# Kernel tuning notes

Hardware: AMD Instinct MI355X
Metric: run time of the kernel (lower is better)

## Reference

```python
import jax, jax.numpy as jnp
import numpy as np

N_SPK, N_UTT, D = 512, 64, 1024
EPS = 1e-6  # matches tf.math.l2_normalize default epsilon guard


def _l2norm(x, axis=-1):
    return x / jnp.sqrt(jnp.maximum(jnp.sum(x * x, axis=axis, keepdims=True), EPS))


def setup_inputs() -> dict:
    key = jax.random.key(0)
    k1, _ = jax.random.split(key)
    inputs = jax.random.normal(k1, (N_SPK, N_UTT, D), dtype=jnp.float32)
    w = jnp.asarray(10.0, dtype=jnp.float32)
    b = jnp.asarray(-5.0, dtype=jnp.float32)
    return {"inputs": inputs, "w": w, "b": b}


def reference(inputs, w, b):
    N, M, _ = inputs.shape
    # speaker centroids: mean over utterances -> [N, D]
    centroids = jnp.mean(inputs, axis=1)
    # utterance (exclusion) centroids: mean of the other M-1 utterances -> [N, M, D]
    ut_centroids = (jnp.sum(inputs, axis=1, keepdims=True) - inputs) / (M - 1)

    e = _l2norm(inputs)          # [N, M, D]
    c = _l2norm(centroids)       # [N, D]
    uc = _l2norm(ut_centroids)   # [N, M, D]

    # cosine sim of every utterance vs every speaker centroid -> [N, M, K]
    cos_all = jnp.einsum('nmd,kd->nmk', e, c)
    # same-speaker entries use the self-exclusion centroid
    cos_self = jnp.sum(e * uc, axis=-1)  # [N, M]
    eye = jnp.eye(N, dtype=inputs.dtype)[:, None, :]  # [N, 1, N]
    cos_sim = cos_all * (1.0 - eye) + cos_self[:, :, None] * eye

    sim = w * cos_sim + b  # [N, M, N]
    # softmax contrastive loss: -S_{j,i,j} + logsumexp_k S_{j,i,k}, summed
    lse = jax.nn.logsumexp(sim, axis=-1)            # [N, M]
    pos = jnp.einsum('nmn->nm', sim)                # diagonal along speaker axes
    loss = jnp.sum(lse - pos)
    return loss
```

## Files before the change

### kernel.cpp

```cpp
#include <hip/hip_runtime.h>
#include <stdint.h>

#define N_SPK 512
#define N_UTT 64
#define DIM   1024
#define NROWS (N_SPK * N_UTT)
#define EPS   1e-6f

#define BM2 256
#define BN2 256
#define BK2 32
#define KT2 (DIM / BK2)

typedef __attribute__((ext_vector_type(8))) short short8;
typedef __attribute__((ext_vector_type(4))) float f32x4;

__device__ __forceinline__ uint16_t f2bf(float f) {
    union { float f; uint32_t i; } un; un.f = f;
    uint32_t x = un.i;
    return (uint16_t)((x + 0x7fffu + ((x >> 16) & 1u)) >> 16);
}

__global__ __launch_bounds__(256) void prep_centroid(
    const float* __restrict__ x, uint16_t* __restrict__ xb,
    uint16_t* __restrict__ cmat, float* __restrict__ xxg,
    float* __restrict__ ssqg)
{
    const int n    = blockIdx.x;
    const int tid  = threadIdx.x;
    const int lane = tid & 63;
    const int w    = tid >> 6;

    const float* xn  = x  + (size_t)n * N_UTT * DIM;
    uint16_t*    xbn = xb + (size_t)n * N_UTT * DIM;

    float Sp[16];
    #pragma unroll
    for (int j = 0; j < 16; ++j) Sp[j] = 0.f;

    #pragma unroll 1
    for (int o = 0; o < 4; ++o) {
        const int m0 = w * 16 + o * 4;

        float4 v[16];
        #pragma unroll
        for (int i = 0; i < 4; ++i)
            #pragma unroll
            for (int j = 0; j < 4; ++j)
                v[i * 4 + j] = *(const float4*)(xn + (size_t)(m0 + i) * DIM + j * 256 + lane * 4);

        float xx[4] = {0.f, 0.f, 0.f, 0.f};
        #pragma unroll
        for (int i = 0; i < 4; ++i) {
            #pragma unroll
            for (int j = 0; j < 4; ++j) {
                const float4 qv = v[i * 4 + j];
                xx[i] += qv.x * qv.x + qv.y * qv.y + qv.z * qv.z + qv.w * qv.w;
                Sp[j * 4 + 0] += qv.x; Sp[j * 4 + 1] += qv.y;
                Sp[j * 4 + 2] += qv.z; Sp[j * 4 + 3] += qv.w;
                ushort4 ov;
                ov.x = f2bf(qv.x); ov.y = f2bf(qv.y); ov.z = f2bf(qv.z); ov.w = f2bf(qv.w);
                *(ushort4*)(xbn + (size_t)(m0 + i) * DIM + j * 256 + lane * 4) = ov;
            }
        }

        #pragma unroll
        for (int i = 0; i < 4; ++i) {
            float t = xx[i];
            #pragma unroll
            for (int off = 1; off < 64; off <<= 1) t += __shfl_xor(t, off);
            if (lane == 0) xxg[n * N_UTT + m0 + i] = t;
        }
    }

    __shared__ float Sh[4][DIM];
    #pragma unroll
    for (int j = 0; j < 4; ++j)
        *(float4*)&Sh[w][j * 256 + lane * 4] =
            make_float4(Sp[j * 4], Sp[j * 4 + 1], Sp[j * 4 + 2], Sp[j * 4 + 3]);
    __syncthreads();

    const int d0 = tid * 4;
    float4 S  = *(const float4*)&Sh[0][d0];
    const float4 b1 = *(const float4*)&Sh[1][d0];
    const float4 b2 = *(const float4*)&Sh[2][d0];
    const float4 b3 = *(const float4*)&Sh[3][d0];
    S.x += b1.x + b2.x + b3.x; S.y += b1.y + b2.y + b3.y;
    S.z += b1.z + b2.z + b3.z; S.w += b1.w + b2.w + b3.w;

    float css = S.x * S.x + S.y * S.y + S.z * S.z + S.w * S.w;
    #pragma unroll
    for (int off = 1; off < 64; off <<= 1) css += __shfl_xor(css, off);
    __shared__ float red[4];
    if ((tid & 63) == 0) red[tid >> 6] = css;
    __syncthreads();
    const float ssq = red[0] + red[1] + red[2] + red[3];

    const float scale = rsqrtf(fmaxf(ssq * (1.0f / 4096.f), EPS)) * (1.0f / 64.f);
    ushort4 oc;
    oc.x = f2bf(S.x * scale); oc.y = f2bf(S.y * scale);
    oc.z = f2bf(S.z * scale); oc.w = f2bf(S.w * scale);
    *(ushort4*)(cmat + (size_t)n * DIM + d0) = oc;
    if (tid == 0) ssqg[n] = ssq;
}

__global__ __launch_bounds__(512, 2) void gemm_lse_kernel(
    const uint16_t* __restrict__ xb, const uint16_t* __restrict__ cmat,
    const float* __restrict__ xxg, const float* __restrict__ ssqg,
    const float* __restrict__ wp, const float* __restrict__ bp,
    float* __restrict__ sumexp2, float* __restrict__ pos)
{
    __shared__ char smem[65536];
    uint16_t* As = (uint16_t*)smem;
    uint16_t* Bs = (uint16_t*)(smem + 32768);
    float*    Se = (float*)smem;

    const int tid   = threadIdx.x;
    const int lane  = tid & 63;
    const int wid   = tid >> 6;
    const int waveM = wid >> 2;
    const int waveN = wid & 3;

    const int bid = blockIdx.x;
    const int rt  = bid & 127;
    const int ct  = bid >> 7;

    const int rowBase = rt * BM2;
    const int colBase = ct * BN2;

    const uint16_t* gAp[2];
    const uint16_t* gBp[2];
    int ldso[2];
    #pragma unroll
    for (int i = 0; i < 2; ++i) {
        const int s    = i * 512 + tid;
        const int srow = s >> 2;
        const int kc   = (s & 3) ^ (srow & 3);
        gAp[i]  = xb   + (size_t)(rowBase + srow) * DIM + kc * 8;
        gBp[i]  = cmat + (size_t)(colBase + srow) * DIM + kc * 8;
        ldso[i] = s * 16;
    }

#define STAGE(buf, ko)                                                          \
    {                                                                           \
        _Pragma("unroll")                                                       \
        for (int i_ = 0; i_ < 2; ++i_) {                                        \
            __builtin_amdgcn_global_load_lds(                                   \
                (const __attribute__((address_space(1))) void*)(gAp[i_] + (ko)),\
                (__attribute__((address_space(3))) void*)(smem + (buf) * 16384 + ldso[i_]), \
                16, 0, 0);                                                      \
            __builtin_amdgcn_global_load_lds(                                   \
                (const __attribute__((address_space(1))) void*)(gBp[i_] + (ko)),\
                (__attribute__((address_space(3))) void*)(smem + 32768 + (buf) * 16384 + ldso[i_]), \
                16, 0, 0);                                                      \
        }                                                                       \
    }

    f32x4 acc[8][4];
    #pragma unroll
    for (int i = 0; i < 8; ++i)
        #pragma unroll
        for (int j = 0; j < 4; ++j)
            acc[i][j] = (f32x4){0.f, 0.f, 0.f, 0.f};

    const int cL = lane & 15;
    const int q  = lane >> 4;

    STAGE(0, 0);
    __syncthreads();

    int cur = 0;
    for (int kt = 0; kt < KT2; ++kt) {
        if (kt + 1 < KT2) STAGE(cur ^ 1, (kt + 1) * BK2);

        const uint16_t* Ab = As + cur * (256 * 32);
        const uint16_t* Bb = Bs + cur * (256 * 32);

        short8 a[8], b[4];
        #pragma unroll
        for (int bi = 0; bi < 8; ++bi) {
            const int row = waveM * 128 + bi * 16 + cL;
            const int ch  = q ^ (row & 3);
            a[bi] = *(const short8*)&Ab[row * 32 + ch * 8];
        }
        #pragma unroll
        for (int bj = 0; bj < 4; ++bj) {
            const int row = waveN * 64 + bj * 16 + cL;
            const int ch  = q ^ (row & 3);
            b[bj] = *(const short8*)&Bb[row * 32 + ch * 8];
        }

        #pragma unroll
        for (int bi = 0; bi < 8; ++bi)
            #pragma unroll
            for (int bj = 0; bj < 4; ++bj)
                acc[bi][bj] = __builtin_amdgcn_mfma_f32_16x16x32_bf16(
                    a[bi], b[bj], acc[bi][bj], 0, 0, 0);

        __syncthreads();
        cur ^= 1;
    }
#undef STAGE

    const float wv = wp[0], bv = bp[0];
    #pragma unroll
    for (int bi = 0; bi < 8; ++bi) {
        #pragma unroll
        for (int r = 0; r < 4; ++r) {
            const int R     = rowBase + waveM * 128 + bi * 16 + q * 4 + r;
            const float xxv = xxg[R];
            const float rn  = rsqrtf(fmaxf(xxv, EPS));
            const int nrow  = R >> 6;
            float s = 0.f;
            #pragma unroll
            for (int bj = 0; bj < 4; ++bj) {
                const int col = colBase + waveN * 64 + bj * 16 + cL;
                const float dot = acc[bi][bj][r];
                float sim;
                if (col == nrow) {
                    const float ssqv = ssqg[nrow];
                    const float xs   = dot * sqrtf(ssqv);
                    const float d2   = ssqv - 2.f * xs + xxv;
                    const float cs   = ((xs - xxv) * (1.f / 63.f)) * rn *
                                       rsqrtf(fmaxf(d2 * (1.f / 3969.f), EPS));
                    sim = wv * cs + bv;
                    pos[R] = sim;
                } else {
                    sim = wv * (dot * rn) + bv;
                }
                s += __expf(sim);
            }
            #pragma unroll
            for (int off = 1; off < 16; off <<= 1) s += __shfl_xor(s, off);
            if (cL == 0)
                Se[waveN * 256 + waveM * 128 + bi * 16 + q * 4 + r] = s;
        }
    }
    __syncthreads();
    if (tid < 256) {
        const float t = Se[tid] + Se[256 + tid] + Se[512 + tid] + Se[768 + tid];
        sumexp2[(size_t)ct * NROWS + rowBase + tid] = t;
    }
}

__global__ __launch_bounds__(256) void finalize_part(
    const float* __restrict__ pos, const float* __restrict__ se2,
    float* __restrict__ partial)
{
    const int tid = threadIdx.x;
    const int r   = blockIdx.x * 256 + tid;
    const float s = se2[r] + se2[NROWS + r];
    float acc = __logf(s) - pos[r];
    #pragma unroll
    for (int off = 1; off < 64; off <<= 1) acc += __shfl_xor(acc, off);
    __shared__ float red[4];
    if ((tid & 63) == 0) red[tid >> 6] = acc;
    __syncthreads();
    if (tid == 0) partial[blockIdx.x] = red[0] + red[1] + red[2] + red[3];
}

__global__ __launch_bounds__(128) void finalize_sum(
    const float* __restrict__ partial, float* __restrict__ out)
{
    const int tid = threadIdx.x;
    float t = partial[tid];
    #pragma unroll
    for (int off = 1; off < 64; off <<= 1) t += __shfl_xor(t, off);
    __shared__ float red[2];
    if ((tid & 63) == 0) red[tid >> 6] = t;
    __syncthreads();
    if (tid == 0) out[0] = red[0] + red[1];
}

extern "C" void kernel_launch(void* const* d_in, const int* in_sizes, int n_in,
                              void* d_out, int out_size, void* d_ws, size_t ws_size,
                              hipStream_t stream)
{
    const float* x  = (const float*)d_in[0];
    const float* wp = (const float*)d_in[1];
    const float* bp = (const float*)d_in[2];
    float* out = (float*)d_out;

    char* ws = (char*)d_ws;
    size_t off = 0;
    uint16_t* xb      = (uint16_t*)(ws + off); off += (size_t)NROWS * DIM * 2;
    uint16_t* cmat    = (uint16_t*)(ws + off); off += (size_t)N_SPK * DIM * 2;
    float*    xxg     = (float*)(ws + off);    off += (size_t)NROWS * 4;
    float*    pos     = (float*)(ws + off);    off += (size_t)NROWS * 4;
    float*    sumexp2 = (float*)(ws + off);    off += (size_t)2 * NROWS * 4;
    float*    ssqg    = (float*)(ws + off);    off += (size_t)N_SPK * 4;
    float*    partial = (float*)(ws + off);    off += (size_t)128 * 4;

    prep_centroid<<<N_SPK, 256, 0, stream>>>(x, xb, cmat, xxg, ssqg);
    gemm_lse_kernel<<<(NROWS / BM2) * (N_SPK / BN2), 512, 0, stream>>>(
        xb, cmat, xxg, ssqg, wp, bp, sumexp2, pos);
    finalize_part<<<NROWS / 256, 256, 0, stream>>>(pos, sumexp2, partial);
    finalize_sum<<<1, 128, 0, stream>>>(partial, out);
}
```

Baseline: 253.5 us.

## Triple-buffer GEMM K-loop with one barrier per step and new LDS swizzle

Replaces the double-buffered K loop, which used two __syncthreads per step, with a three-slot LDS ring. Loads are issued two tiles ahead and each step waits with a partial vmcnt followed by a single barrier. The LDS XOR swizzle changes to use (row>>1)&3 to reduce bank conflicts, and MFMA blocks are raised with s_setprio. LDS per block grows from 64KB to 96KB, which may not allow two blocks per CU as launch_bounds(512,2) requests, so occupancy could drop.

```diff
diff --git a/kernel.cpp b/kernel.cpp
--- a/kernel.cpp
+++ b/kernel.cpp
@@ -110,10 +110,8 @@
     const float* __restrict__ wp, const float* __restrict__ bp,
     float* __restrict__ sumexp2, float* __restrict__ pos)
 {
-    __shared__ char smem[65536];
-    uint16_t* As = (uint16_t*)smem;
-    uint16_t* Bs = (uint16_t*)(smem + 32768);
-    float*    Se = (float*)smem;
+    __shared__ char smem[98304];
+    float* Se = (float*)smem;
 
     const int tid   = threadIdx.x;
     const int lane  = tid & 63;
@@ -135,23 +133,24 @@
     for (int i = 0; i < 2; ++i) {
         const int s    = i * 512 + tid;
         const int srow = s >> 2;
-        const int kc   = (s & 3) ^ (srow & 3);
+        const int kc   = (s & 3) ^ ((srow >> 1) & 3);
         gAp[i]  = xb   + (size_t)(rowBase + srow) * DIM + kc * 8;
         gBp[i]  = cmat + (size_t)(colBase + srow) * DIM + kc * 8;
         ldso[i] = s * 16;
     }
 
-#define STAGE(buf, ko)                                                          \
+#define STAGE(slot, kt_)                                                        \
     {                                                                           \
+        const int ko_ = (kt_) * BK2;                                            \
         _Pragma("unroll")                                                       \
         for (int i_ = 0; i_ < 2; ++i_) {                                        \
             __builtin_amdgcn_global_load_lds(                                   \
-                (const __attribute__((address_space(1))) void*)(gAp[i_] + (ko)),\
-                (__attribute__((address_space(3))) void*)(smem + (buf) * 16384 + ldso[i_]), \
+                (const __attribute__((address_space(1))) void*)(gAp[i_] + ko_), \
+                (__attribute__((address_space(3))) void*)(smem + (slot) * 16384 + ldso[i_]), \
                 16, 0, 0);                                                      \
             __builtin_amdgcn_global_load_lds(                                   \
-                (const __attribute__((address_space(1))) void*)(gBp[i_] + (ko)),\
-                (__attribute__((address_space(3))) void*)(smem + 32768 + (buf) * 16384 + ldso[i_]), \
+                (const __attribute__((address_space(1))) void*)(gBp[i_] + ko_), \
+                (__attribute__((address_space(3))) void*)(smem + 49152 + (slot) * 16384 + ldso[i_]), \
                 16, 0, 0);                                                      \
         }                                                                       \
     }
@@ -163,45 +162,64 @@
         for (int j = 0; j < 4; ++j)
             acc[i][j] = (f32x4){0.f, 0.f, 0.f, 0.f};
 
-    const int cL = lane & 15;
-    const int q  = lane >> 4;
+    const int cL  = lane & 15;
+    const int q   = lane >> 4;
+    const int kcs = q ^ ((cL >> 1) & 3);
+
+#define COMPUTE(slot_)                                                          \
+    {                                                                           \
+        const uint16_t* Ab_ = (const uint16_t*)(smem + (slot_) * 16384);        \
+        const uint16_t* Bb_ = (const uint16_t*)(smem + 49152 + (slot_) * 16384);\
+        short8 a_[8], b_[4];                                                    \
+        _Pragma("unroll")                                                       \
+        for (int bi_ = 0; bi_ < 8; ++bi_)                                       \
+            a_[bi_] = *(const short8*)&Ab_[(waveM * 128 + bi_ * 16 + cL) * 32 + kcs * 8]; \
+        _Pragma("unroll")                                                       \
+        for (int bj_ = 0; bj_ < 4; ++bj_)                                       \
+            b_[bj_] = *(const short8*)&Bb_[(waveN * 64 + bj_ * 16 + cL) * 32 + kcs * 8]; \
+        __builtin_amdgcn_s_setprio(1);                                          \
+        _Pragma("unroll")                                                       \
+        for (int bi_ = 0; bi_ < 8; ++bi_)                                       \
+            _Pragma("unroll")                                                   \
+            for (int bj_ = 0; bj_ < 4; ++bj_)                                   \
+                acc[bi_][bj_] = __builtin_amdgcn_mfma_f32_16x16x32_bf16(        \
+                    a_[bi_], b_[bj_], acc[bi_][bj_], 0, 0, 0);                  \
+        __builtin_amdgcn_s_setprio(0);                                          \
+    }
+
+#define ITER(kt_, cSlot, sSlot)                                                 \
+    {                                                                           \
+        asm volatile("s_waitcnt vmcnt(4)" ::: "memory");                        \
+        __builtin_amdgcn_sched_barrier(0);                                      \
+        __builtin_amdgcn_s_barrier();                                           \
+        __builtin_amdgcn_sched_barrier(0);                                      \
+        STAGE(sSlot, (kt_) + 2);                                                \
+        COMPUTE(cSlot);                                                         \
+    }
 
     STAGE(0, 0);
-    __syncthreads();
-
-    int cur = 0;
-    for (int kt = 0; kt < KT2; ++kt) {
-        if (kt + 1 < KT2) STAGE(cur ^ 1, (kt + 1) * BK2);
-
-        const uint16_t* Ab = As + cur * (256 * 32);
-        const uint16_t* Bb = Bs + cur * (256 * 32);
-
-        short8 a[8], b[4];
-        #pragma unroll
-        for (int bi = 0; bi < 8; ++bi) {
-            const int row = waveM * 128 + bi * 16 + cL;
-            const int ch  = q ^ (row & 3);
-            a[bi] = *(const short8*)&Ab[row * 32 + ch * 8];
-        }
-        #pragma unroll
-        for (int bj = 0; bj < 4; ++bj) {
-            const int row = waveN * 64 + bj * 16 + cL;
-            const int ch  = q ^ (row & 3);
-            b[bj] = *(const short8*)&Bb[row * 32 + ch * 8];
-        }
-
-        #pragma unroll
-        for (int bi = 0; bi < 8; ++bi)
-            #pragma unroll
-            for (int bj = 0; bj < 4; ++bj)
-                acc[bi][bj] = __builtin_amdgcn_mfma_f32_16x16x32_bf16(
-                    a[bi], b[bj], acc[bi][bj], 0, 0, 0);
-
-        __syncthreads();
-        cur ^= 1;
-    }
+    STAGE(1, 1);
+
+    for (int tb = 0; tb < 30; tb += 3) {
+        ITER(tb + 0, 0, 2);
+        ITER(tb + 1, 1, 0);
+        ITER(tb + 2, 2, 1);
+    }
+    asm volatile("s_waitcnt vmcnt(4)" ::: "memory");
+    __builtin_amdgcn_sched_barrier(0);
+    __builtin_amdgcn_s_barrier();
+    __builtin_amdgcn_sched_barrier(0);
+    COMPUTE(0);
+    asm volatile("s_waitcnt vmcnt(0)" ::: "memory");
+    __builtin_amdgcn_sched_barrier(0);
+    __builtin_amdgcn_s_barrier();
+    __builtin_amdgcn_sched_barrier(0);
+    COMPUTE(1);
 #undef STAGE
-
+#undef COMPUTE
+#undef ITER
+
+    __syncthreads();
     const float wv = wp[0], bv = bp[0];
     #pragma unroll
     for (int bi = 0; bi < 8; ++bi) {
```

Measured after the change: 250.8 us. No clear change (-1.0%).

## Restructure GEMM main loop with BK=64, interleaved staging and MFMA priority scheduling

Applied to the files above, without the earlier changes.

Doubles the K tile to 64 with a 128 KB double-buffered LDS layout using an 8-way XOR swizzle. Each K tile is split into four MFMA phases, with async global-to-LDS loads for the next tile issued between them, separated by scheduling barriers and raised wave priority around MFMA blocks. The aim is to halve the number of barrier/wait rounds and overlap memory traffic with matrix math. The cost is more LDS per block, which likely lowers occupancy to one block per CU, plus extra fine-grained barriers.

```diff
diff --git a/kernel.cpp b/kernel.cpp
--- a/kernel.cpp
+++ b/kernel.cpp
@@ -9,8 +9,8 @@
 
 #define BM2 256
 #define BN2 256
-#define BK2 32
-#define KT2 (DIM / BK2)
+#define BK3 64
+#define KT3 (DIM / BK3)
 
 typedef __attribute__((ext_vector_type(8))) short short8;
 typedef __attribute__((ext_vector_type(4))) float f32x4;
@@ -110,10 +110,8 @@
     const float* __restrict__ wp, const float* __restrict__ bp,
     float* __restrict__ sumexp2, float* __restrict__ pos)
 {
-    __shared__ char smem[65536];
-    uint16_t* As = (uint16_t*)smem;
-    uint16_t* Bs = (uint16_t*)(smem + 32768);
-    float*    Se = (float*)smem;
+    __shared__ char smem[131072];
+    float* Se = (float*)smem;
 
     const int tid   = threadIdx.x;
     const int lane  = tid & 63;
@@ -128,33 +126,28 @@
     const int rowBase = rt * BM2;
     const int colBase = ct * BN2;
 
-    const uint16_t* gAp[2];
-    const uint16_t* gBp[2];
-    int ldso[2];
+    int aoff[2];
+    int ldsb[2];
     #pragma unroll
     for (int i = 0; i < 2; ++i) {
-        const int s    = i * 512 + tid;
-        const int srow = s >> 2;
-        const int kc   = (s & 3) ^ (srow & 3);
-        gAp[i]  = xb   + (size_t)(rowBase + srow) * DIM + kc * 8;
-        gBp[i]  = cmat + (size_t)(colBase + srow) * DIM + kc * 8;
-        ldso[i] = s * 16;
-    }
-
-#define STAGE(buf, ko)                                                          \
-    {                                                                           \
-        _Pragma("unroll")                                                       \
-        for (int i_ = 0; i_ < 2; ++i_) {                                        \
-            __builtin_amdgcn_global_load_lds(                                   \
-                (const __attribute__((address_space(1))) void*)(gAp[i_] + (ko)),\
-                (__attribute__((address_space(3))) void*)(smem + (buf) * 16384 + ldso[i_]), \
-                16, 0, 0);                                                      \
-            __builtin_amdgcn_global_load_lds(                                   \
-                (const __attribute__((address_space(1))) void*)(gBp[i_] + (ko)),\
-                (__attribute__((address_space(3))) void*)(smem + 32768 + (buf) * 16384 + ldso[i_]), \
-                16, 0, 0);                                                      \
-        }                                                                       \
-    }
+        const int s   = tid + i * 512;
+        const int row = s >> 3;
+        const int c   = (s & 7) ^ (row & 7);
+        aoff[i] = row * 1024 + c * 8;
+        ldsb[i] = s * 16;
+    }
+    const uint16_t* Abase = xb   + (size_t)rowBase * DIM;
+    const uint16_t* Bbase = cmat + (size_t)colBase * DIM;
+
+#define STAGEH(matBase, ldsMatOff, buf, h, kt_)                                 \
+    { _Pragma("unroll")                                                         \
+      for (int i_ = 0; i_ < 2; ++i_) {                                          \
+        __builtin_amdgcn_global_load_lds(                                       \
+            (const __attribute__((address_space(1))) void*)(                    \
+                (matBase) + (size_t)(h) * 131072 + (kt_) * 64 + aoff[i_]),      \
+            (__attribute__((address_space(3))) void*)(                          \
+                smem + (ldsMatOff) + (buf) * 32768 + (h) * 16384 + ldsb[i_]),   \
+            16, 0, 0); } }
 
     f32x4 acc[8][4];
     #pragma unroll
@@ -163,45 +156,85 @@
         for (int j = 0; j < 4; ++j)
             acc[i][j] = (f32x4){0.f, 0.f, 0.f, 0.f};
 
-    const int cL = lane & 15;
-    const int q  = lane >> 4;
-
-    STAGE(0, 0);
-    __syncthreads();
-
-    int cur = 0;
-    for (int kt = 0; kt < KT2; ++kt) {
-        if (kt + 1 < KT2) STAGE(cur ^ 1, (kt + 1) * BK2);
-
-        const uint16_t* Ab = As + cur * (256 * 32);
-        const uint16_t* Bb = Bs + cur * (256 * 32);
-
-        short8 a[8], b[4];
-        #pragma unroll
-        for (int bi = 0; bi < 8; ++bi) {
-            const int row = waveM * 128 + bi * 16 + cL;
-            const int ch  = q ^ (row & 3);
-            a[bi] = *(const short8*)&Ab[row * 32 + ch * 8];
-        }
-        #pragma unroll
-        for (int bj = 0; bj < 4; ++bj) {
-            const int row = waveN * 64 + bj * 16 + cL;
-            const int ch  = q ^ (row & 3);
-            b[bj] = *(const short8*)&Bb[row * 32 + ch * 8];
-        }
-
-        #pragma unroll
-        for (int bi = 0; bi < 8; ++bi)
-            #pragma unroll
-            for (int bj = 0; bj < 4; ++bj)
-                acc[bi][bj] = __builtin_amdgcn_mfma_f32_16x16x32_bf16(
-                    a[bi], b[bj], acc[bi][bj], 0, 0, 0);
-
-        __syncthreads();
-        cur ^= 1;
-    }
-#undef STAGE
-
+    const int cL  = lane & 15;
+    const int q   = lane >> 4;
+    const int pk0 = ((q ^ (cL & 7)) * 16);
+
+#define READ_A(buf, bi0, pk, dest)                                              \
+    { const char* Ab_ = smem + (buf) * 32768 + waveM * 16384;                   \
+      _Pragma("unroll")                                                         \
+      for (int i_ = 0; i_ < 4; ++i_)                                            \
+        dest[i_] = *(const short8*)(Ab_ + ((bi0) + i_) * 2048 + cL * 128 + (pk)); }
+
+#define READ_B(buf, pk, dest)                                                   \
+    { const char* Bb_ = smem + 65536 + (buf) * 32768 + (waveN >> 1) * 16384;    \
+      _Pragma("unroll")                                                         \
+      for (int j_ = 0; j_ < 4; ++j_)                                            \
+        dest[j_] = *(const short8*)(Bb_ + ((waveN & 1) * 64 + j_ * 16 + cL) * 128 + (pk)); }
+
+#define MFMA16(bi0, av, bv)                                                     \
+    { __builtin_amdgcn_s_setprio(1);                                            \
+      _Pragma("unroll")                                                         \
+      for (int i_ = 0; i_ < 4; ++i_)                                            \
+        _Pragma("unroll")                                                       \
+        for (int j_ = 0; j_ < 4; ++j_)                                          \
+          acc[(bi0) + i_][j_] = __builtin_amdgcn_mfma_f32_16x16x32_bf16(        \
+              av[i_], bv[j_], acc[(bi0) + i_][j_], 0, 0, 0);                    \
+      __builtin_amdgcn_s_setprio(0); }
+
+#define SBAR()  { __builtin_amdgcn_sched_barrier(0);                            \
+                  __builtin_amdgcn_s_barrier();                                 \
+                  __builtin_amdgcn_sched_barrier(0); }
+
+#define KTILE(buf, kt_, DO_STAGE)                                               \
+    {                                                                           \
+        asm volatile("s_waitcnt vmcnt(0)" ::: "memory");                        \
+        SBAR();                                                                 \
+        short8 a0[4], a1[4], b0[4], b1[4];                                      \
+                             \
+        READ_A(buf, 0, pk0, a0); READ_B(buf, pk0, b0);                          \
+        if (DO_STAGE) { STAGEH(Abase, 0, (buf) ^ 1, 0, (kt_) + 1);              \
+                        STAGEH(Abase, 0, (buf) ^ 1, 1, (kt_) + 1); }            \
+        SBAR();                                                                 \
+        MFMA16(0, a0, b0);                                                      \
+        SBAR();                                                                 \
+                             \
+        READ_A(buf, 4, pk0, a1);                                                \
+        if (DO_STAGE) { STAGEH(Bbase, 65536, (buf) ^ 1, 0, (kt_) + 1);          \
+                        STAGEH(Bbase, 65536, (buf) ^ 1, 1, (kt_) + 1); }        \
+        SBAR();                                                                 \
+        MFMA16(4, a1, b0);                                                      \
+        SBAR();                                                                 \
+                                                     \
+        READ_A(buf, 0, pk0 ^ 64, a0); READ_B(buf, pk0 ^ 64, b1);                \
+        SBAR();                                                                 \
+        MFMA16(0, a0, b1);                                                      \
+        SBAR();                                                                 \
+                                                     \
+        READ_A(buf, 4, pk0 ^ 64, a1);                                           \
+        SBAR();                                                                 \
+        MFMA16(4, a1, b1);                                                      \
+                               \
+    }
+
+    STAGEH(Abase, 0, 0, 0, 0); STAGEH(Abase, 0, 0, 1, 0);
+    STAGEH(Bbase, 65536, 0, 0, 0); STAGEH(Bbase, 65536, 0, 1, 0);
+
+    #pragma unroll 1
+    for (int ktp = 0; ktp < KT3 - 2; ktp += 2) {
+        KTILE(0, ktp, 1);
+        KTILE(1, ktp + 1, 1);
+    }
+    KTILE(0, KT3 - 2, 1);
+    KTILE(1, KT3 - 1, 0);
+#undef STAGEH
+#undef READ_A
+#undef READ_B
+#undef MFMA16
+#undef SBAR
+#undef KTILE
+
+    __syncthreads();
     const float wv = wp[0], bv = bp[0];
     #pragma unroll
     for (int bi = 0; bi < 8; ++bi) {
```

New measurement: 248.3 us. 2.0% less time.
